# Kernel optimization log

Measured on AMD Instinct MI355X. Metric: run time of the kernel, lower is better.

## Reference

```python
import jax, jax.numpy as jnp
import numpy as np

B = 8192
D1 = 1024
D2 = 1024
H = 4096  # subnet hidden width
SCALE_LIMIT = 1.0


def _mlp(x, W1, b1, W2, b2):
    # Linear -> ReLU -> Linear
    return jnp.maximum(x @ W1 + b1, 0.0) @ W2 + b2


def setup_inputs() -> dict:
    key = jax.random.key(0)
    ks = jax.random.split(key, 17)
    inp = {"x": jax.random.normal(ks[0], (B, D1 + D2), dtype=jnp.float32)}
    # four subnets: s1,t1 map d2->d1 ; s2,t2 map d1->d2
    specs = {"s1": (D2, D1), "t1": (D2, D1), "s2": (D1, D2), "t2": (D1, D2)}
    i = 1
    for name, (din, dout) in specs.items():
        inp[f"{name}_W1"] = 0.02 * jax.random.normal(ks[i], (din, H), dtype=jnp.float32); i += 1
        inp[f"{name}_b1"] = jnp.zeros((H,), dtype=jnp.float32)
        inp[f"{name}_W2"] = 0.02 * jax.random.normal(ks[i], (H, dout), dtype=jnp.float32); i += 1
        inp[f"{name}_b2"] = jnp.zeros((dout,), dtype=jnp.float32)
    return inp


def reference(x,
              s1_W1, s1_b1, s1_W2, s1_b2,
              t1_W1, t1_b1, t1_W2, t1_b2,
              s2_W1, s2_b1, s2_W2, s2_b2,
              t2_W1, t2_b1, t2_W2, t2_b2):
    x1, x2 = x[:, :D1], x[:, D1:]
    # first half-step: update x1 conditioned on x2
    s2v = jnp.tanh(_mlp(x2, s1_W1, s1_b1, s1_W2, s1_b2)) * SCALE_LIMIT  # [B, D1]
    t2v = _mlp(x2, t1_W1, t1_b1, t1_W2, t1_b2)                          # [B, D1]
    y1 = x1 * jnp.exp(s2v) + t2v
    # second half-step: update x2 conditioned on y1
    s1v = jnp.tanh(_mlp(y1, s2_W1, s2_b1, s2_W2, s2_b2)) * SCALE_LIMIT  # [B, D2]
    t1v = _mlp(y1, t2_W1, t2_b1, t2_W2, t2_b2)                          # [B, D2]
    y2 = x2 * jnp.exp(s1v) + t1v
    y = jnp.concatenate([y1, y2], axis=1)  # [B, D1+D2]
    # exact triangular-coupling log-det (what the autograd loop computes per-sample)
    log_det = jnp.sum(s2v, axis=1) + jnp.sum(s1v, axis=1)  # [B]
    return y, log_det
```

## Files before the change

kernel.cpp:

```cpp
#include <hip/hip_runtime.h>
#include <cstdint>
#include <cstddef>

#define BDIM 8192
#define D1 1024
#define HDIM 4096

typedef __attribute__((ext_vector_type(8))) short short8;
typedef __attribute__((ext_vector_type(4))) float f32x4;
typedef __attribute__((ext_vector_type(4))) unsigned short u16x4;

__device__ inline void async_load16(const void* g, void* l) {
  __builtin_amdgcn_global_load_lds(
      (const __attribute__((address_space(1))) void*)g,
      (__attribute__((address_space(3))) void*)l,
      16 , 0 , 0 );
}

__device__ inline unsigned short f2bf(float f) {
  union { float f; uint32_t u; } v; v.f = f;
  uint32_t u = v.u;
  uint32_t r = u + 0x7FFFu + ((u >> 16) & 1u);
  return (unsigned short)(r >> 16);
}
__device__ inline float bf2f(unsigned short u) {
  union { uint32_t u; float f; } v; v.u = (uint32_t)u << 16; return v.f;
}

__global__ __launch_bounds__(512, 2)
void gemm8(const unsigned short* __restrict__ A0,
           const unsigned short* __restrict__ A1, int lda,
           const unsigned short* __restrict__ B0,
           const unsigned short* __restrict__ B1,
           const float* __restrict__ bias0, const float* __restrict__ bias1,
           unsigned short* __restrict__ C0, unsigned short* __restrict__ C1,
           int ldc, int K, int relu) {
  __shared__ __align__(16) unsigned short smem[65536];

  const int z = blockIdx.z;
  const unsigned short* A  = z ? A1 : A0;
  const unsigned short* Bw = z ? B1 : B0;
  const float* biasP       = z ? bias1 : bias0;
  unsigned short* C        = z ? C1 : C0;

  const int nX  = gridDim.x;
  const int nwg = gridDim.x * gridDim.y;
  const int bid = blockIdx.y * gridDim.x + blockIdx.x;
  const int q = nwg >> 3, r = nwg & 7;
  const int xcd = bid & 7, rest = bid >> 3;
  const int wg = (xcd < r ? xcd * (q + 1) : r * (q + 1) + (xcd - r) * q) + rest;
  const int tm = wg / nX, tn = wg % nX;
  const int m0 = tm * 256, n0 = tn * 256;

  const int tid  = threadIdx.x;
  const int wave = tid >> 6, lane = tid & 63;
  const int quad = lane >> 4, l15 = lane & 15;
  const int wm = wave >> 2, wn = wave & 3;

  const int sr    = tid >> 2;
  const int sslot = (tid & 3) ^ ((tid >> 3) & 3);
  const unsigned short* gA = A  + (long)(m0 + sr) * lda + sslot * 8;
  const unsigned short* gB = Bw + (long)(n0 + sr) * K   + sslot * 8;

  const int swz = ((quad ^ ((l15 >> 1) & 3)) << 3);
  const unsigned short* aB = smem + wm * 4096  + l15 * 32 + swz;
  const unsigned short* bB = smem + 32768 + wn * 2048 + l15 * 32 + swz;

  f32x4 acc[8][4] = {};
  const int NT = K >> 6;

#define STAGE_A(NB, SL, KT) { \
  unsigned short* lw = smem + (NB)*16384 + (SL)*8192 + wave*512; \
  const unsigned short* g = gA + (long)(KT)*64 + (SL)*32; \
  async_load16(g, lw); \
  async_load16(g + 128*(long)lda, lw + 4096); }

#define STAGE_B(NB, SL, KT) { \
  unsigned short* lw = smem + 32768 + (NB)*16384 + (SL)*8192 + wave*512; \
  const unsigned short* g = gB + (long)(KT)*64 + (SL)*32; \
  async_load16(g, lw); \
  async_load16(g + 128*(long)K, lw + 4096); }

#define READ_A(dst, BUF, SL, MH) { \
  const unsigned short* p = aB + (BUF)*16384 + (SL)*8192 + (MH)*2048; \
  dst[0] = *(const short8*)(p);        dst[1] = *(const short8*)(p + 512); \
  dst[2] = *(const short8*)(p + 1024); dst[3] = *(const short8*)(p + 1536); }

#define READ_B(dst, BUF, SL) { \
  const unsigned short* p = bB + (BUF)*16384 + (SL)*8192; \
  dst[0] = *(const short8*)(p);        dst[1] = *(const short8*)(p + 512); \
  dst[2] = *(const short8*)(p + 1024); dst[3] = *(const short8*)(p + 1536); }

#define MFMA16(MH, AV, BV) \
  _Pragma("unroll") \
  for (int mt = 0; mt < 4; ++mt) { \
    _Pragma("unroll") \
    for (int nt = 0; nt < 4; ++nt) { \
      acc[(MH)*4 + mt][nt] = __builtin_amdgcn_mfma_f32_16x16x32_bf16( \
          AV[mt], BV[nt], acc[(MH)*4 + mt][nt], 0, 0, 0); \
    } }

#define BARRIER() asm volatile("s_barrier" ::: "memory")
#define VMCNT4()  asm volatile("s_waitcnt vmcnt(4)" ::: "memory")

#define TILE_BODY(BUF, NB, TNX) { \
  short8 a0[4], a1[4], b0v[4], b1v[4]; \
   \
  READ_A(a0, BUF, 0, 0); READ_B(b0v, BUF, 0); \
  STAGE_A(NB, 0, TNX); \
  BARRIER(); \
  __builtin_amdgcn_s_setprio(1); MFMA16(0, a0, b0v); __builtin_amdgcn_s_setprio(0); \
   \
  READ_A(a1, BUF, 0, 1); \
  STAGE_B(NB, 0, TNX); \
  VMCNT4(); \
  BARRIER(); \
  __builtin_amdgcn_s_setprio(1); MFMA16(1, a1, b0v); __builtin_amdgcn_s_setprio(0); \
   \
  READ_A(a0, BUF, 1, 0); READ_B(b1v, BUF, 1); \
  STAGE_A(NB, 1, TNX); \
  BARRIER(); \
  __builtin_amdgcn_s_setprio(1); MFMA16(0, a0, b1v); __builtin_amdgcn_s_setprio(0); \
   \
  READ_A(a1, BUF, 1, 1); \
  STAGE_B(NB, 1, TNX); \
  VMCNT4(); \
  BARRIER(); \
  __builtin_amdgcn_s_setprio(1); MFMA16(1, a1, b1v); __builtin_amdgcn_s_setprio(0); \
}

  STAGE_A(0, 0, 0); STAGE_B(0, 0, 0); STAGE_A(0, 1, 0); STAGE_B(0, 1, 0);
  VMCNT4();
  BARRIER();

#pragma unroll 1
  for (int t = 0; t < NT; t += 2) {
    const int tnx1 = t + 1;
    const int tnx2 = (t + 2 < NT) ? t + 2 : NT - 1;
    TILE_BODY(0, 1, tnx1);
    TILE_BODY(1, 0, tnx2);
  }

  asm volatile("s_waitcnt vmcnt(0)" ::: "memory");
  BARRIER();

  unsigned short* sc = smem + wave * 8192;
#pragma unroll
  for (int nt = 0; nt < 4; ++nt) {
    const int col = n0 + wn * 64 + nt * 16 + l15;
    const float bv = biasP[col];
#pragma unroll
    for (int mt = 0; mt < 8; ++mt) {
#pragma unroll
      for (int rr = 0; rr < 4; ++rr) {
        const int lrow = mt * 16 + quad * 4 + rr;
        float v = acc[mt][nt][rr] + bv;
        if (relu) v = v > 0.f ? v : 0.f;
        sc[lrow * 64 + ((nt * 16 + l15) ^ (((lrow >> 2) & 3) << 4))] = f2bf(v);
      }
    }
  }
  const long rowbase = m0 + wm * 128;
  const int colbase  = n0 + wn * 64;
#pragma unroll
  for (int i = 0; i < 16; ++i) {
    const int L   = i * 1024 + lane * 16;
    const int row = L >> 7;
    const int sp  = (L & 127) >> 4;
    const int cg  = sp ^ ((((row) >> 2) & 3) << 1);
    short8 v = *(const short8*)&sc[row * 64 + sp * 8];
    *(short8*)&C[(rowbase + row) * (long)ldc + colbase + cg * 8] = v;
  }

#undef STAGE_A
#undef STAGE_B
#undef READ_A
#undef READ_B
#undef MFMA16
#undef BARRIER
#undef VMCNT4
#undef TILE_BODY
}

__global__ __launch_bounds__(256)
void couple(const unsigned short* sb, const unsigned short* __restrict__ tb,
            const float* __restrict__ x, float* __restrict__ y,
            unsigned short* y1b, float* __restrict__ ld,
            long growoff, int xoff, int addld) {
  __shared__ float wsum[4];
  const int row = blockIdx.x;
  const long grow = growoff + row;
  const int c = threadIdx.x * 4;

  u16x4 sv4 = *(const u16x4*)&sb[(long)row * 1024 + c];
  u16x4 tv4 = *(const u16x4*)&tb[(long)row * 1024 + c];
  f32x4 xv  = *(const f32x4*)&x[grow * 2048 + xoff + c];
  f32x4 yv;
  unsigned short yb[4];
  float rs = 0.f;
#pragma unroll
  for (int j = 0; j < 4; ++j) {
    float s  = bf2f(sv4[j]);
    float t  = bf2f(tv4[j]);
    float sv = tanhf(s);
    rs += sv;
    float yy = xv[j] * __expf(sv) + t;
    yv[j] = yy;
    yb[j] = f2bf(yy);
  }
  *(f32x4*)&y[grow * 2048 + xoff + c] = yv;
  if (y1b) {
    u16x4 o; o[0] = yb[0]; o[1] = yb[1]; o[2] = yb[2]; o[3] = yb[3];
    *(u16x4*)&y1b[(long)row * 1024 + c] = o;
  }
#pragma unroll
  for (int o = 32; o > 0; o >>= 1) rs += __shfl_down(rs, o);
  const int wv = threadIdx.x >> 6, ln = threadIdx.x & 63;
  if (ln == 0) wsum[wv] = rs;
  __syncthreads();
  if (threadIdx.x == 0) {
    float tot = wsum[0] + wsum[1] + wsum[2] + wsum[3];
    if (addld) ld[grow] += tot; else ld[grow] = tot;
  }
}

__global__ __launch_bounds__(256)
void transpose_cast(const float* __restrict__ in, unsigned short* __restrict__ out,
                    int R, int C) {
  __shared__ float tile[32][33];
  const int bx = blockIdx.x * 32;
  const int by = blockIdx.y * 32;
  const int tx = threadIdx.x & 31;
  const int ty = threadIdx.x >> 5;
  for (int j = ty; j < 32; j += 8)
    tile[j][tx] = in[(long)(by + j) * C + bx + tx];
  __syncthreads();
  for (int j = ty; j < 32; j += 8)
    out[(long)(bx + j) * R + by + tx] = f2bf(tile[tx][j]);
}

__global__ __launch_bounds__(256)
void cast_x2(const float* __restrict__ x, unsigned short* __restrict__ x2b) {
  long i = (long)blockIdx.x * 256 + threadIdx.x;
  long row = i >> 10, col = i & 1023;
  x2b[i] = f2bf(x[row * (2 * D1) + D1 + col]);
}

extern "C" void kernel_launch(void* const* d_in, const int* in_sizes, int n_in,
                              void* d_out, int out_size, void* d_ws, size_t ws_size,
                              hipStream_t stream) {
  const float* x     = (const float*)d_in[0];
  const float* s1_W1 = (const float*)d_in[1];
  const float* s1_b1 = (const float*)d_in[2];
  const float* s1_W2 = (const float*)d_in[3];
  const float* s1_b2 = (const float*)d_in[4];
  const float* t1_W1 = (const float*)d_in[5];
  const float* t1_b1 = (const float*)d_in[6];
  const float* t1_W2 = (const float*)d_in[7];
  const float* t1_b2 = (const float*)d_in[8];
  const float* s2_W1 = (const float*)d_in[9];
  const float* s2_b1 = (const float*)d_in[10];
  const float* s2_W2 = (const float*)d_in[11];
  const float* s2_b2 = (const float*)d_in[12];
  const float* t2_W1 = (const float*)d_in[13];
  const float* t2_b1 = (const float*)d_in[14];
  const float* t2_W2 = (const float*)d_in[15];
  const float* t2_b2 = (const float*)d_in[16];

  const size_t MB = 1024UL * 1024UL;
  float* y_out  = (float*)d_out;
  float* ld_out = (float*)d_out + (long)BDIM * (2 * D1);
  char* ws = (char*)d_ws;

  if (ws_size >= 192 * MB) {
    unsigned short* w1a = (unsigned short*)(ws + 0 * MB);
    unsigned short* w1b = (unsigned short*)(ws + 8 * MB);
    unsigned short* w2a = (unsigned short*)(ws + 16 * MB);
    unsigned short* w2b = (unsigned short*)(ws + 24 * MB);
    unsigned short* x2b = (unsigned short*)(ws + 32 * MB);
    unsigned short* tb  = (unsigned short*)(ws + 48 * MB);
    unsigned short* h   = (unsigned short*)(ws + 64 * MB);

    cast_x2<<<(BDIM * D1) / 256, 256, 0, stream>>>(x, x2b);
    transpose_cast<<<dim3(HDIM / 32, D1 / 32), 256, 0, stream>>>(s1_W1, w1a, D1, HDIM);
    transpose_cast<<<dim3(HDIM / 32, D1 / 32), 256, 0, stream>>>(t1_W1, w1b, D1, HDIM);
    transpose_cast<<<dim3(D1 / 32, HDIM / 32), 256, 0, stream>>>(s1_W2, w2a, HDIM, D1);
    transpose_cast<<<dim3(D1 / 32, HDIM / 32), 256, 0, stream>>>(t1_W2, w2b, HDIM, D1);

    gemm8<<<dim3(16, 32, 2), 512, 0, stream>>>(x2b, x2b, D1, w1a, w1b,
        s1_b1, t1_b1, h, h + 4096, 2 * HDIM, D1, 1);
    transpose_cast<<<dim3(HDIM / 32, D1 / 32), 256, 0, stream>>>(s2_W1, w1a, D1, HDIM);
    transpose_cast<<<dim3(HDIM / 32, D1 / 32), 256, 0, stream>>>(t2_W1, w1b, D1, HDIM);
    gemm8<<<dim3(4, 32, 2), 512, 0, stream>>>(h, h + 4096, 2 * HDIM, w2a, w2b,
        s1_b2, t1_b2, x2b , tb, D1, HDIM, 0);
    transpose_cast<<<dim3(D1 / 32, HDIM / 32), 256, 0, stream>>>(s2_W2, w2a, HDIM, D1);
    transpose_cast<<<dim3(D1 / 32, HDIM / 32), 256, 0, stream>>>(t2_W2, w2b, HDIM, D1);
    couple<<<BDIM, 256, 0, stream>>>(x2b, tb, x, y_out, x2b ,
                                     ld_out, 0, 0, 0);
    gemm8<<<dim3(16, 32, 2), 512, 0, stream>>>(x2b, x2b, D1, w1a, w1b,
        s2_b1, t2_b1, h, h + 4096, 2 * HDIM, D1, 1);
    gemm8<<<dim3(4, 32, 2), 512, 0, stream>>>(h, h + 4096, 2 * HDIM, w2a, w2b,
        s2_b2, t2_b2, x2b , tb, D1, HDIM, 0);
    couple<<<BDIM, 256, 0, stream>>>(x2b, tb, x, y_out, nullptr, ld_out, 0, D1, 1);
  } else {
    int NC = 2;
    while (NC < 16) {
      size_t need = 80 * MB + (16 * MB) / NC + (128 * MB) / NC;
      if (need <= ws_size) break;
      NC <<= 1;
    }
    const int Mrows = BDIM / NC;
    unsigned short* w1s1 = (unsigned short*)(ws + 0 * MB);
    unsigned short* w1t1 = (unsigned short*)(ws + 8 * MB);
    unsigned short* w1s2 = (unsigned short*)(ws + 16 * MB);
    unsigned short* w1t2 = (unsigned short*)(ws + 24 * MB);
    unsigned short* w2s1 = (unsigned short*)(ws + 32 * MB);
    unsigned short* w2t1 = (unsigned short*)(ws + 40 * MB);
    unsigned short* w2s2 = (unsigned short*)(ws + 48 * MB);
    unsigned short* w2t2 = (unsigned short*)(ws + 56 * MB);
    unsigned short* x2b  = (unsigned short*)(ws + 64 * MB);
    unsigned short* tb   = (unsigned short*)(ws + 80 * MB);
    unsigned short* h    = (unsigned short*)(ws + 80 * MB + (16 * MB) / NC);

    cast_x2<<<(BDIM * D1) / 256, 256, 0, stream>>>(x, x2b);
    transpose_cast<<<dim3(HDIM / 32, D1 / 32), 256, 0, stream>>>(s1_W1, w1s1, D1, HDIM);
    transpose_cast<<<dim3(HDIM / 32, D1 / 32), 256, 0, stream>>>(t1_W1, w1t1, D1, HDIM);
    transpose_cast<<<dim3(HDIM / 32, D1 / 32), 256, 0, stream>>>(s2_W1, w1s2, D1, HDIM);
    transpose_cast<<<dim3(HDIM / 32, D1 / 32), 256, 0, stream>>>(t2_W1, w1t2, D1, HDIM);
    transpose_cast<<<dim3(D1 / 32, HDIM / 32), 256, 0, stream>>>(s1_W2, w2s1, HDIM, D1);
    transpose_cast<<<dim3(D1 / 32, HDIM / 32), 256, 0, stream>>>(t1_W2, w2t1, HDIM, D1);
    transpose_cast<<<dim3(D1 / 32, HDIM / 32), 256, 0, stream>>>(s2_W2, w2s2, HDIM, D1);
    transpose_cast<<<dim3(D1 / 32, HDIM / 32), 256, 0, stream>>>(t2_W2, w2t2, HDIM, D1);

    for (int c = 0; c < NC; ++c) {
      const long moff = (long)c * Mrows;
      unsigned short* xA = x2b + moff * D1;
      gemm8<<<dim3(16, Mrows / 256, 2), 512, 0, stream>>>(xA, xA, D1, w1s1, w1t1,
          s1_b1, t1_b1, h, h + 4096, 2 * HDIM, D1, 1);
      gemm8<<<dim3(4, Mrows / 256, 2), 512, 0, stream>>>(h, h + 4096, 2 * HDIM,
          w2s1, w2t1, s1_b2, t1_b2, xA, tb, D1, HDIM, 0);
      couple<<<Mrows, 256, 0, stream>>>(xA, tb, x, y_out, xA, ld_out, moff, 0, 0);
      gemm8<<<dim3(16, Mrows / 256, 2), 512, 0, stream>>>(xA, xA, D1, w1s2, w1t2,
          s2_b1, t2_b1, h, h + 4096, 2 * HDIM, D1, 1);
      gemm8<<<dim3(4, Mrows / 256, 2), 512, 0, stream>>>(h, h + 4096, 2 * HDIM,
          w2s2, w2t2, s2_b2, t2_b2, xA, tb, D1, HDIM, 0);
      couple<<<Mrows, 256, 0, stream>>>(xA, tb, x, y_out, nullptr, ld_out, moff, D1, 1);
    }
  }
}
```

Before: 763.7 us.

## Deepen GEMM LDS pipeline to four K32 stages and batch weight transposes

```diff
diff --git a/kernel.cpp b/kernel.cpp
--- a/kernel.cpp
+++ b/kernel.cpp
@@ -62,83 +62,86 @@
   const unsigned short* gA = A  + (long)(m0 + sr) * lda + sslot * 8;
   const unsigned short* gB = Bw + (long)(n0 + sr) * K   + sslot * 8;
 
-  const int swz = ((quad ^ ((l15 >> 1) & 3)) << 3);
-  const unsigned short* aB = smem + wm * 4096  + l15 * 32 + swz;
-  const unsigned short* bB = smem + 32768 + wn * 2048 + l15 * 32 + swz;
+  const int rdoff = l15 * 32 + ((quad ^ ((l15 >> 1) & 3)) << 3);
 
   f32x4 acc[8][4] = {};
-  const int NT = K >> 6;
-
-#define STAGE_A(NB, SL, KT) { \
-  unsigned short* lw = smem + (NB)*16384 + (SL)*8192 + wave*512; \
-  const unsigned short* g = gA + (long)(KT)*64 + (SL)*32; \
+  const int NT = K >> 5;
+
+#define STAGE_A(SB, KT) { \
+  unsigned short* lw = smem + (SB)*8192 + wave*512; \
+  const unsigned short* g = gA + (long)(KT)*32; \
   async_load16(g, lw); \
   async_load16(g + 128*(long)lda, lw + 4096); }
 
-#define STAGE_B(NB, SL, KT) { \
-  unsigned short* lw = smem + 32768 + (NB)*16384 + (SL)*8192 + wave*512; \
-  const unsigned short* g = gB + (long)(KT)*64 + (SL)*32; \
+#define STAGE_B(SB, KT) { \
+  unsigned short* lw = smem + 32768 + (SB)*8192 + wave*512; \
+  const unsigned short* g = gB + (long)(KT)*32; \
   async_load16(g, lw); \
   async_load16(g + 128*(long)K, lw + 4096); }
 
-#define READ_A(dst, BUF, SL, MH) { \
-  const unsigned short* p = aB + (BUF)*16384 + (SL)*8192 + (MH)*2048; \
-  dst[0] = *(const short8*)(p);        dst[1] = *(const short8*)(p + 512); \
-  dst[2] = *(const short8*)(p + 1024); dst[3] = *(const short8*)(p + 1536); }
-
-#define READ_B(dst, BUF, SL) { \
-  const unsigned short* p = bB + (BUF)*16384 + (SL)*8192; \
-  dst[0] = *(const short8*)(p);        dst[1] = *(const short8*)(p + 512); \
-  dst[2] = *(const short8*)(p + 1024); dst[3] = *(const short8*)(p + 1536); }
-
-#define MFMA16(MH, AV, BV) \
+#define READ_AL(d, BUF) { \
+  const unsigned short* p = smem + (BUF)*8192 + wm*4096 + rdoff; \
+  d[0] = *(const short8*)(p);        d[1] = *(const short8*)(p + 512); \
+  d[2] = *(const short8*)(p + 1024); d[3] = *(const short8*)(p + 1536); }
+
+#define READ_AH(d, BUF) { \
+  const unsigned short* p = smem + (BUF)*8192 + wm*4096 + 2048 + rdoff; \
+  d[0] = *(const short8*)(p);        d[1] = *(const short8*)(p + 512); \
+  d[2] = *(const short8*)(p + 1024); d[3] = *(const short8*)(p + 1536); }
+
+#define READ_B(d, BUF) { \
+  const unsigned short* p = smem + 32768 + (BUF)*8192 + wn*2048 + rdoff; \
+  d[0] = *(const short8*)(p);        d[1] = *(const short8*)(p + 512); \
+  d[2] = *(const short8*)(p + 1024); d[3] = *(const short8*)(p + 1536); }
+
+#define MFMA16L(AV, BV) \
   _Pragma("unroll") \
   for (int mt = 0; mt < 4; ++mt) { \
     _Pragma("unroll") \
     for (int nt = 0; nt < 4; ++nt) { \
-      acc[(MH)*4 + mt][nt] = __builtin_amdgcn_mfma_f32_16x16x32_bf16( \
-          AV[mt], BV[nt], acc[(MH)*4 + mt][nt], 0, 0, 0); \
+      acc[mt][nt] = __builtin_amdgcn_mfma_f32_16x16x32_bf16( \
+          AV[mt], BV[nt], acc[mt][nt], 0, 0, 0); \
     } }
 
+#define MFMA16H(AV, BV) \
+  _Pragma("unroll") \
+  for (int mt = 0; mt < 4; ++mt) { \
+    _Pragma("unroll") \
+    for (int nt = 0; nt < 4; ++nt) { \
+      acc[4 + mt][nt] = __builtin_amdgcn_mfma_f32_16x16x32_bf16( \
+          AV[mt], BV[nt], acc[4 + mt][nt], 0, 0, 0); \
+    } }
+
 #define BARRIER() asm volatile("s_barrier" ::: "memory")
-#define VMCNT4()  asm volatile("s_waitcnt vmcnt(4)" ::: "memory")
-
-#define TILE_BODY(BUF, NB, TNX) { \
-  short8 a0[4], a1[4], b0v[4], b1v[4]; \
-   \
-  READ_A(a0, BUF, 0, 0); READ_B(b0v, BUF, 0); \
-  STAGE_A(NB, 0, TNX); \
+#define VMCNT8()  asm volatile("s_waitcnt vmcnt(8)" ::: "memory")
+
+#define STEP(BUF, SB, KTS, CA, CB, NA, NBv) { \
+  short8 h4[4]; \
+  READ_AH(h4, BUF); \
+  { const int kt = (KTS) < NT ? (KTS) : NT - 1; \
+    STAGE_A(SB, kt); STAGE_B(SB, kt); } \
+  __builtin_amdgcn_s_setprio(1); MFMA16L(CA, CB); __builtin_amdgcn_s_setprio(0); \
+  VMCNT8(); \
   BARRIER(); \
-  __builtin_amdgcn_s_setprio(1); MFMA16(0, a0, b0v); __builtin_amdgcn_s_setprio(0); \
-   \
-  READ_A(a1, BUF, 0, 1); \
-  STAGE_B(NB, 0, TNX); \
-  VMCNT4(); \
-  BARRIER(); \
-  __builtin_amdgcn_s_setprio(1); MFMA16(1, a1, b0v); __builtin_amdgcn_s_setprio(0); \
-   \
-  READ_A(a0, BUF, 1, 0); READ_B(b1v, BUF, 1); \
-  STAGE_A(NB, 1, TNX); \
-  BARRIER(); \
-  __builtin_amdgcn_s_setprio(1); MFMA16(0, a0, b1v); __builtin_amdgcn_s_setprio(0); \
-   \
-  READ_A(a1, BUF, 1, 1); \
-  STAGE_B(NB, 1, TNX); \
-  VMCNT4(); \
-  BARRIER(); \
-  __builtin_amdgcn_s_setprio(1); MFMA16(1, a1, b1v); __builtin_amdgcn_s_setprio(0); \
-}
-
-  STAGE_A(0, 0, 0); STAGE_B(0, 0, 0); STAGE_A(0, 1, 0); STAGE_B(0, 1, 0);
-  VMCNT4();
+  READ_AL(NA, ((BUF) + 1) & 3); READ_B(NBv, ((BUF) + 1) & 3); \
+  __builtin_amdgcn_s_setprio(1); MFMA16H(h4, CB); __builtin_amdgcn_s_setprio(0); \
+}
+
+  short8 pa[4], pb[4], qa[4], qb[4];
+
+  STAGE_A(0, 0); STAGE_B(0, 0);
+  STAGE_A(1, 1); STAGE_B(1, 1);
+  STAGE_A(2, 2); STAGE_B(2, 2);
+  VMCNT8();
   BARRIER();
+  READ_AL(pa, 0); READ_B(pb, 0);
 
 #pragma unroll 1
-  for (int t = 0; t < NT; t += 2) {
-    const int tnx1 = t + 1;
-    const int tnx2 = (t + 2 < NT) ? t + 2 : NT - 1;
-    TILE_BODY(0, 1, tnx1);
-    TILE_BODY(1, 0, tnx2);
+  for (int t = 0; t < NT; t += 4) {
+    STEP(0, 3, t + 3, pa, pb, qa, qb);
+    STEP(1, 0, t + 4, qa, qb, pa, pb);
+    STEP(2, 1, t + 5, pa, pb, qa, qb);
+    STEP(3, 2, t + 6, qa, qb, pa, pb);
   }
 
   asm volatile("s_waitcnt vmcnt(0)" ::: "memory");
@@ -174,12 +177,14 @@
 
 #undef STAGE_A
 #undef STAGE_B
-#undef READ_A
+#undef READ_AL
+#undef READ_AH
 #undef READ_B
-#undef MFMA16
+#undef MFMA16L
+#undef MFMA16H
 #undef BARRIER
-#undef VMCNT4
-#undef TILE_BODY
+#undef VMCNT8
+#undef STEP
 }
 
 __global__ __launch_bounds__(256)
@@ -225,9 +230,15 @@
 }
 
 __global__ __launch_bounds__(256)
-void transpose_cast(const float* __restrict__ in, unsigned short* __restrict__ out,
-                    int R, int C) {
+void transpose_cast4(const float* __restrict__ s0, const float* __restrict__ s1,
+                     const float* __restrict__ s2, const float* __restrict__ s3,
+                     unsigned short* __restrict__ d0, unsigned short* __restrict__ d1,
+                     unsigned short* __restrict__ d2, unsigned short* __restrict__ d3,
+                     int R, int C) {
   __shared__ float tile[32][33];
+  const int bz = blockIdx.z;
+  const float* in = bz == 0 ? s0 : bz == 1 ? s1 : bz == 2 ? s2 : s3;
+  unsigned short* out = bz == 0 ? d0 : bz == 1 ? d1 : bz == 2 ? d2 : d3;
   const int bx = blockIdx.x * 32;
   const int by = blockIdx.y * 32;
   const int tx = threadIdx.x & 31;
@@ -282,19 +293,19 @@
     unsigned short* h   = (unsigned short*)(ws + 64 * MB);
 
     cast_x2<<<(BDIM * D1) / 256, 256, 0, stream>>>(x, x2b);
-    transpose_cast<<<dim3(HDIM / 32, D1 / 32), 256, 0, stream>>>(s1_W1, w1a, D1, HDIM);
-    transpose_cast<<<dim3(HDIM / 32, D1 / 32), 256, 0, stream>>>(t1_W1, w1b, D1, HDIM);
-    transpose_cast<<<dim3(D1 / 32, HDIM / 32), 256, 0, stream>>>(s1_W2, w2a, HDIM, D1);
-    transpose_cast<<<dim3(D1 / 32, HDIM / 32), 256, 0, stream>>>(t1_W2, w2b, HDIM, D1);
+    transpose_cast4<<<dim3(HDIM / 32, D1 / 32, 2), 256, 0, stream>>>(
+        s1_W1, t1_W1, s1_W1, s1_W1, w1a, w1b, w1a, w1a, D1, HDIM);
+    transpose_cast4<<<dim3(D1 / 32, HDIM / 32, 2), 256, 0, stream>>>(
+        s1_W2, t1_W2, s1_W2, s1_W2, w2a, w2b, w2a, w2a, HDIM, D1);
 
     gemm8<<<dim3(16, 32, 2), 512, 0, stream>>>(x2b, x2b, D1, w1a, w1b,
         s1_b1, t1_b1, h, h + 4096, 2 * HDIM, D1, 1);
-    transpose_cast<<<dim3(HDIM / 32, D1 / 32), 256, 0, stream>>>(s2_W1, w1a, D1, HDIM);
-    transpose_cast<<<dim3(HDIM / 32, D1 / 32), 256, 0, stream>>>(t2_W1, w1b, D1, HDIM);
+    transpose_cast4<<<dim3(HDIM / 32, D1 / 32, 2), 256, 0, stream>>>(
+        s2_W1, t2_W1, s2_W1, s2_W1, w1a, w1b, w1a, w1a, D1, HDIM);
     gemm8<<<dim3(4, 32, 2), 512, 0, stream>>>(h, h + 4096, 2 * HDIM, w2a, w2b,
         s1_b2, t1_b2, x2b , tb, D1, HDIM, 0);
-    transpose_cast<<<dim3(D1 / 32, HDIM / 32), 256, 0, stream>>>(s2_W2, w2a, HDIM, D1);
-    transpose_cast<<<dim3(D1 / 32, HDIM / 32), 256, 0, stream>>>(t2_W2, w2b, HDIM, D1);
+    transpose_cast4<<<dim3(D1 / 32, HDIM / 32, 2), 256, 0, stream>>>(
+        s2_W2, t2_W2, s2_W2, s2_W2, w2a, w2b, w2a, w2a, HDIM, D1);
     couple<<<BDIM, 256, 0, stream>>>(x2b, tb, x, y_out, x2b ,
                                      ld_out, 0, 0, 0);
     gemm8<<<dim3(16, 32, 2), 512, 0, stream>>>(x2b, x2b, D1, w1a, w1b,
@@ -323,14 +334,10 @@
     unsigned short* h    = (unsigned short*)(ws + 80 * MB + (16 * MB) / NC);
 
     cast_x2<<<(BDIM * D1) / 256, 256, 0, stream>>>(x, x2b);
-    transpose_cast<<<dim3(HDIM / 32, D1 / 32), 256, 0, stream>>>(s1_W1, w1s1, D1, HDIM);
-    transpose_cast<<<dim3(HDIM / 32, D1 / 32), 256, 0, stream>>>(t1_W1, w1t1, D1, HDIM);
-    transpose_cast<<<dim3(HDIM / 32, D1 / 32), 256, 0, stream>>>(s2_W1, w1s2, D1, HDIM);
-    transpose_cast<<<dim3(HDIM / 32, D1 / 32), 256, 0, stream>>>(t2_W1, w1t2, D1, HDIM);
-    transpose_cast<<<dim3(D1 / 32, HDIM / 32), 256, 0, stream>>>(s1_W2, w2s1, HDIM, D1);
-    transpose_cast<<<dim3(D1 / 32, HDIM / 32), 256, 0, stream>>>(t1_W2, w2t1, HDIM, D1);
-    transpose_cast<<<dim3(D1 / 32, HDIM / 32), 256, 0, stream>>>(s2_W2, w2s2, HDIM, D1);
-    transpose_cast<<<dim3(D1 / 32, HDIM / 32), 256, 0, stream>>>(t2_W2, w2t2, HDIM, D1);
+    transpose_cast4<<<dim3(HDIM / 32, D1 / 32, 4), 256, 0, stream>>>(
+        s1_W1, t1_W1, s2_W1, t2_W1, w1s1, w1t1, w1s2, w1t2, D1, HDIM);
+    transpose_cast4<<<dim3(D1 / 32, HDIM / 32, 4), 256, 0, stream>>>(
+        s1_W2, t1_W2, s2_W2, t2_W2, w2s1, w2t1, w2s2, w2t2, HDIM, D1);
 
     for (int c = 0; c < NC; ++c) {
       const long moff = (long)c * Mrows;
```

Result: slower. 784.1 us (+2.7%).
